# Optimization experiments

Hardware: AMD Instinct MI355X
Metric: run time of the kernel (lower is better)

The kernel has to match this reference:

```python
import jax, jax.numpy as jnp
import numpy as np

HID = 256
NL = 4
NC = 5
SPACE = 16


def _grid_sample(feat, grid):
    # feat [B,C,H,W]; grid [B,Hg,Wg,2] in [-1,1]; bilinear, align_corners=True, zeros padding
    B, C, H, W = feat.shape
    x = (grid[..., 0] + 1.0) * 0.5 * (W - 1)
    y = (grid[..., 1] + 1.0) * 0.5 * (H - 1)
    x0f = jnp.floor(x)
    y0f = jnp.floor(y)
    wx1 = x - x0f
    wy1 = y - y0f

    def corner(yf, xf, wgt):
        valid = (xf >= 0) & (xf <= W - 1) & (yf >= 0) & (yf <= H - 1)
        xi = jnp.clip(xf, 0, W - 1).astype(jnp.int32)
        yi = jnp.clip(yf, 0, H - 1).astype(jnp.int32)
        v = jax.vmap(lambda f, yy, xx: f[:, yy, xx])(feat, yi, xi)  # [B,C,Hg,Wg]
        return v * (wgt * valid.astype(feat.dtype))[:, None]

    return (corner(y0f, x0f, (1 - wy1) * (1 - wx1))
            + corner(y0f, x0f + 1, (1 - wy1) * wx1)
            + corner(y0f + 1, x0f, wy1 * (1 - wx1))
            + corner(y0f + 1, x0f + 1, wy1 * wx1))


def _conv(x, w, b, pad):
    y = jax.lax.conv_general_dilated(x, w, (1, 1), ((pad, pad), (pad, pad)),
                                     dimension_numbers=('NCHW', 'OIHW', 'NCHW'))
    return y + b[None, :, None, None]


def _resize_ac(x, oh, ow):
    # bilinear resize with align_corners=True
    B, C, H, W = x.shape
    ys = jnp.linspace(0.0, H - 1.0, oh)
    xs = jnp.linspace(0.0, W - 1.0, ow)
    y0 = jnp.floor(ys).astype(jnp.int32)
    y1 = jnp.minimum(y0 + 1, H - 1)
    x0 = jnp.floor(xs).astype(jnp.int32)
    x1 = jnp.minimum(x0 + 1, W - 1)
    wy = (ys - y0)[None, None, :, None]
    wx = (xs - x0)[None, None, None, :]
    top = x[:, :, y0, :] * (1 - wy) + x[:, :, y1, :] * wy
    return top[:, :, :, x0] * (1 - wx) + top[:, :, :, x1] * wx


def _mlp(x, w1, b1, w2, b2):
    # 2-layer MLP, dropout is identity at inference
    return jax.nn.relu(x @ w1 + b1) @ w2 + b2


def setup_inputs() -> dict:
    key = jax.random.key(0)
    ks = jax.random.split(key, 16)
    B, H, W = 8, 512, 512

    def rn(k, shape, s=0.02):
        return jax.random.normal(k, shape, jnp.float32) * s

    return {
        'images': jax.random.normal(ks[0], (B, 3, H, W), jnp.float32),
        'feat0': jax.random.normal(ks[1], (B, HID, 128, 128), jnp.float32),
        'feat1': jax.random.normal(ks[2], (B, HID, 64, 64), jnp.float32),
        'feat2': jax.random.normal(ks[3], (B, HID, 32, 32), jnp.float32),
        'feat3': jax.random.normal(ks[4], (B, HID, 16, 16), jnp.float32),
        'mask_feat': jax.random.normal(ks[5], (B, HID, 128, 128), jnp.float32),
        'o': jax.random.normal(ks[6], (B, 16, 16, 768), jnp.float32),
        'dw1': rn(ks[7], (768, HID)), 'db1': jnp.zeros((HID,), jnp.float32),
        'dw2': rn(ks[8], (HID, 8)), 'db2': jnp.zeros((8,), jnp.float32),
        'cw1': rn(ks[9], (HID, HID)), 'cb1': jnp.zeros((HID,), jnp.float32),
        'cw2': rn(ks[10], (HID, NC + 1)), 'cb2': jnp.zeros((NC + 1,), jnp.float32),
        'conv_w': rn(ks[11], (HID, HID * NL, 3, 3)), 'conv_b': jnp.zeros((HID,), jnp.float32),
        'mw1': rn(ks[12], (HID, HID, 3, 3)), 'mb1': jnp.zeros((HID,), jnp.float32),
        'bn_g': jnp.ones((HID,), jnp.float32), 'bn_b': jnp.zeros((HID,), jnp.float32),
        'bn_m': jnp.zeros((HID,), jnp.float32), 'bn_v': jnp.ones((HID,), jnp.float32),
        'mw2': rn(ks[13], (1, HID, 1, 1)), 'mb2': jnp.zeros((1,), jnp.float32),
    }


def reference(images, feat0, feat1, feat2, feat3, mask_feat, o,
              dw1, db1, dw2, db2, cw1, cb1, cw2, cb2, conv_w, conv_b,
              mw1, mb1, bn_g, bn_b, bn_m, bn_v, mw2, mb2):
    B, _, H, W = images.shape
    ny = int(np.ceil(H / SPACE))
    nx = int(np.ceil(W / SPACE))
    # AnchorPoints: meshgrid 'xy', scaled by space, shifted by half-cell origin
    gx, gy = jnp.meshgrid(jnp.arange(nx, dtype=jnp.float32), jnp.arange(ny, dtype=jnp.float32))
    origin = jnp.array([(W % SPACE) or SPACE, (H % SPACE) or SPACE], jnp.float32) / 2
    anchors = jnp.stack([gx, gy], -1) * SPACE + origin  # [ny,nx,2] (x,y)

    # learned offsets: MLP then pixel-shuffle style 16x16x8 -> 32x32x2
    d = _mlp(o, dw1, db1, dw2, db2)  # [B,16,16,8]
    d = d.reshape(B, 16, 16, 2, 2, 2).transpose(0, 1, 3, 2, 4, 5).reshape(B, 32, 32, 2)
    prop = anchors[None] + d  # deformed proposals [B,32,32,2]

    feats = [feat0, feat1, feat2, feat3]
    strides = [4, 8, 16, 32]
    rois = []
    for f, s in zip(feats, strides):
        fh, fw = f.shape[2], f.shape[3]
        grid = 2.0 * prop / s / jnp.array([fw, fh], jnp.float32) - 1.0
        rois.append(_grid_sample(f, grid))
    roi = jnp.concatenate(rois, 1)  # [B, HID*NL, 32, 32]
    roi = _conv(roi, conv_w, conv_b, 1).transpose(0, 2, 3, 1)  # [B,32,32,HID]
    logits = _mlp(roi, cw1, cb1, cw2, cb2)  # [B,32,32,NC+1]

    # mask head: conv3x3 -> BN(eval) -> ReLU -> conv1x1(pad=1) -> bilinear upsample (align_corners=True)
    m = _conv(mask_feat, mw1, mb1, 1)
    m = m * (bn_g * jax.lax.rsqrt(bn_v + 1e-5))[None, :, None, None] \
        + (bn_b - bn_m * bn_g * jax.lax.rsqrt(bn_v + 1e-5))[None, :, None, None]
    m = jax.nn.relu(m)
    m = _conv(m, mw2, mb2, 1)  # 1x1 conv with padding=1 -> [B,1,130,130] (as in source)
    masks = _resize_ac(m, H, W)  # [B,1,H,W]

    return (prop.reshape(B, -1, 2), logits.reshape(B, -1, NC + 1), masks)
```

## Files before the change

### kernel.cpp

```cpp
#include <hip/hip_runtime.h>
#include <hip/hip_bf16.h>
#include <cstdint>
#include <cstddef>

using bf16x8 = __attribute__((ext_vector_type(8))) short;
using f32x4  = __attribute__((ext_vector_type(4))) float;

static constexpr size_t ROI_OFF  = 0;
static constexpr size_t ROI_N    = (size_t)8 * 1024 * 32 * 32;
static constexpr size_t PART_OFF = ROI_OFF + ROI_N;
static constexpr size_t PART_N   = (size_t)4 * 8192 * 256;
static constexpr size_t WT_OFF   = PART_OFF + PART_N;
static constexpr size_t WTR_SH   = (size_t)294912 * 8;
static constexpr size_t WTM_SH   = (size_t)73728 * 8;
static constexpr size_t M2P_OFF  = WT_OFF + (WTR_SH + WTM_SH) / 2;
static constexpr size_t M2P_N    = (size_t)2 * 8 * 130 * 130;

__device__ __forceinline__ uint32_t pk2(float a, float b) {
  __hip_bfloat162 h = __float22bfloat162_rn(make_float2(a, b));
  union { __hip_bfloat162 h; uint32_t u; } c; c.h = h;
  return c.u;
}

__device__ __forceinline__ void gld16(const void* g, void* l) {
  __builtin_amdgcn_global_load_lds(
      (const __attribute__((address_space(1))) void*)g,
      (__attribute__((address_space(3))) void*)l, 16, 0, 0);
}

__global__ __launch_bounds__(256) void k_prep_w(
    const float* __restrict__ conv_w, const float* __restrict__ mw1,
    short* __restrict__ wTr, short* __restrict__ wTm) {
  __shared__ float sm[16 * 292];
  int t = threadIdx.x;
  int bid = blockIdx.x;
  bool is_m = (bid >= 512);
  int b2 = is_m ? (bid - 512) : bid;
  int kidx = is_m ? (b2 & 7) : (b2 & 31);
  int cog  = is_m ? (b2 >> 3) : (b2 >> 5);
  const float* src = is_m ? mw1 : conv_w;
  short* dst = is_m ? wTm : wTr;
  int CI = is_m ? 256 : 1024;
  int ci0 = kidx * 32;
  int co0 = cog * 16;
  for (int e = t; e < 4608; e += 256) {
    int row = e / 288, pos = e - row * 288;
    sm[row * 292 + pos] = src[((size_t)(co0 + row) * CI + ci0) * 9 + pos];
  }
  __syncthreads();
  int nb = cog >> 3, cofrag = cog & 7;
  for (int e = t; e < 576; e += 256) {
    int tap = e >> 6, kg = (e >> 4) & 3, lr = e & 15;
    float v[8];
#pragma unroll
    for (int j = 0; j < 8; ++j) v[j] = sm[lr * 292 + (kg * 8 + j) * 9 + tap];
    uint4 pk = make_uint4(pk2(v[0], v[1]), pk2(v[2], v[3]),
                          pk2(v[4], v[5]), pk2(v[6], v[7]));
    size_t chunk = ((size_t)(kidx * 2 + nb) * 9 + tap) * 512
                 + cofrag * 64 + kg * 16 + lr;
    *(uint4*)&dst[chunk * 8] = pk;
  }
}

__global__ __launch_bounds__(256) void k_prop(
    const float* __restrict__ o,
    const float* __restrict__ dw1, const float* __restrict__ db1,
    const float* __restrict__ dw2, const float* __restrict__ db2,
    float* __restrict__ prop) {
  __shared__ float o_lds[4 * 768];
  __shared__ float h_lds[4 * 256];
  int t = threadIdx.x;
  int bid = blockIdx.x;
  int b = bid >> 6;
  int rem = bid & 63;
  int i = rem >> 2;
  int j0 = (rem & 3) * 4;
  const float* obase = o + ((size_t)(b * 16 + i) * 16 + j0) * 768;
  for (int e = t; e < 4 * 768; e += 256) o_lds[e] = obase[e];
  __syncthreads();
  float h0 = 0.f, h1 = 0.f, h2 = 0.f, h3 = 0.f;
  for (int k = 0; k < 768; ++k) {
    float w = dw1[k * 256 + t];
    h0 = fmaf(o_lds[k], w, h0);
    h1 = fmaf(o_lds[768 + k], w, h1);
    h2 = fmaf(o_lds[1536 + k], w, h2);
    h3 = fmaf(o_lds[2304 + k], w, h3);
  }
  float bb = db1[t];
  h_lds[t]        = fmaxf(h0 + bb, 0.f);
  h_lds[256 + t]  = fmaxf(h1 + bb, 0.f);
  h_lds[512 + t]  = fmaxf(h2 + bb, 0.f);
  h_lds[768 + t]  = fmaxf(h3 + bb, 0.f);
  __syncthreads();
  if (t < 32) {
    int pos = t >> 3;
    int c   = t & 7;
    float acc = db2[c];
    const float* hp = h_lds + pos * 256;
    for (int k = 0; k < 256; ++k) acc = fmaf(hp[k], dw2[k * 8 + c], acc);
    int p = c >> 2, q = (c >> 1) & 1, cc = c & 1;
    int row = 2 * i + p;
    int col = 2 * (j0 + pos) + q;
    float anchor = (cc == 0) ? ((float)col * 16.f + 8.f) : ((float)row * 16.f + 8.f);
    prop[((size_t)(b * 32 + row) * 32 + col) * 2 + cc] = anchor + acc;
  }
}

__global__ __launch_bounds__(256) void k_sample(
    const float* __restrict__ f0, const float* __restrict__ f1,
    const float* __restrict__ f2, const float* __restrict__ f3,
    const float* __restrict__ prop, float* __restrict__ roi) {
  int py = blockIdx.x;
  int l  = blockIdx.y;
  int b  = blockIdx.z;
  int t  = threadIdx.x;
  int xq = t & 31;
  int cq = t >> 5;
  const float* f = (l == 0) ? f0 : (l == 1) ? f1 : (l == 2) ? f2 : f3;
  int fsz = 128 >> l;
  float s = (float)(4 << l);

  size_t pidx = ((size_t)b * 32 + py) * 32 + xq;
  float px = prop[pidx * 2 + 0];
  float pv = prop[pidx * 2 + 1];
  float gx = 2.f * px / s / (float)fsz - 1.f;
  float gy = 2.f * pv / s / (float)fsz - 1.f;
  float x = (gx + 1.f) * 0.5f * (float)(fsz - 1);
  float y = (gy + 1.f) * 0.5f * (float)(fsz - 1);
  float x0f = floorf(x), y0f = floorf(y);
  float wx1 = x - x0f, wy1 = y - y0f;

  int off[4];
  float wgt[4];
#pragma unroll
  for (int cy = 0; cy < 2; ++cy) {
#pragma unroll
    for (int cx = 0; cx < 2; ++cx) {
      float xf = x0f + (float)cx;
      float yf = y0f + (float)cy;
      float w = (cy ? wy1 : (1.f - wy1)) * (cx ? wx1 : (1.f - wx1));
      bool valid = (xf >= 0.f) && (xf <= (float)(fsz - 1)) &&
                   (yf >= 0.f) && (yf <= (float)(fsz - 1));
      int xi = (int)fminf(fmaxf(xf, 0.f), (float)(fsz - 1));
      int yi = (int)fminf(fmaxf(yf, 0.f), (float)(fsz - 1));
      off[cy * 2 + cx] = yi * fsz + xi;
      wgt[cy * 2 + cx] = valid ? w : 0.f;
    }
  }
  const float* fb = f + (size_t)b * 256 * fsz * fsz;
  float* rb = roi + ((size_t)b * 1024 + l * 256) * 1024 + py * 32 + xq;
  for (int c0 = 0; c0 < 256; c0 += 8) {
    int c = c0 + cq;
    const float* fc = fb + (size_t)c * fsz * fsz;
    float acc = wgt[0] * fc[off[0]] + wgt[1] * fc[off[1]] +
                wgt[2] * fc[off[2]] + wgt[3] * fc[off[3]];
    rb[(size_t)c * 1024] = acc;
  }
}

__global__ __launch_bounds__(512, 2) void k_roi_mfma(
    const float* __restrict__ roi, const short* __restrict__ wTr,
    float* __restrict__ part) {
  __shared__ short A_s[2][340 * 32];
  __shared__ short B_s[4608 * 8];
  int t = threadIdx.x;
  int lane = t & 63, wv = t >> 6, wm = wv >> 1, wn = wv & 1;
  int kg = lane >> 4, lr = lane & 15;
  int bid = blockIdx.x;
  int nb = bid & 1;
  int mi = (bid >> 1) & 31;
  int b = mi >> 2, yt = mi & 3;
  int ks = bid >> 6;

  f32x4 acc[4][4];
#pragma unroll
  for (int m = 0; m < 4; ++m)
#pragma unroll
    for (int n = 0; n < 4; ++n) acc[m][n] = {0.f, 0.f, 0.f, 0.f};

  float ld[3][8];
  auto stage_load = [&](int kc) {
#pragma unroll
    for (int i = 0; i < 3; ++i) {
      int e = i * 512 + t;
      bool on = e < 1360;
      int ee = on ? e : 0;
      int px = ee % 340;
      int cg = ee / 340;
      int r = px / 34;
      int x = px - r * 34 - 1;
      int y = yt * 8 + r - 1;
      bool ok = on && (x >= 0) && (x < 32) && (y >= 0) && (y < 32);
      const float* src = roi + (((size_t)(b * 1024 + ks * 256 + kc * 32 + cg * 8)) << 10)
                             + y * 32 + x;
#pragma unroll
      for (int j = 0; j < 8; ++j) ld[i][j] = ok ? src[j << 10] : 0.f;
    }
  };
  auto stage_write = [&](int buf) {
#pragma unroll
    for (int i = 0; i < 3; ++i) {
      int e = i * 512 + t;
      if (e < 1360) {
        int px = e % 340;
        int cg = e / 340;
        uint4 pk = make_uint4(pk2(ld[i][0], ld[i][1]), pk2(ld[i][2], ld[i][3]),
                              pk2(ld[i][4], ld[i][5]), pk2(ld[i][6], ld[i][7]));
        *(uint4*)&A_s[buf][px * 32 + (((cg ^ (px >> 1)) & 3) << 3)] = pk;
      }
    }
  };
  auto issue_h1 = [&](int kc) {
    const short* s = wTr + ((size_t)((ks * 8 + kc) * 2 + nb) * 4608) * 8;
    for (int w = wv; w < 40; w += 8)
      gld16(s + ((size_t)w * 64 + lane) * 8, &B_s[w * 512]);
  };
  auto issue_h2 = [&](int kc) {
    const short* s = wTr + (((size_t)((ks * 8 + kc) * 2 + nb) * 4608 + 2560)) * 8;
    for (int w = wv; w < 32; w += 8)
      gld16(s + ((size_t)w * 64 + lane) * 8, &B_s[2560 * 8 + w * 512]);
  };

#define ROI_TAPS(T0, T1)                                                          \
  {                                                                               \
    _Pragma("unroll")                                                             \
    for (int tap = (T0); tap < (T1); ++tap) {                                     \
      int ky = tap / 3, kx = tap - ky * 3;                                        \
      bf16x8 bfr[4];                                                              \
      _Pragma("unroll")                                                           \
      for (int n = 0; n < 4; ++n)                                                 \
        bfr[n] = *(const bf16x8*)&B_s[((((tap * 8 + wn * 4 + n) * 4 + kg) * 16)   \
                                       + lr) * 8];                                \
      _Pragma("unroll")                                                           \
      for (int m = 0; m < 4; ++m) {                                               \
        int pb = wm * 64 + m * 16;                                                \
        int px = ((pb >> 5) + ky) * 34 + (pb & 31) + lr + kx;                     \
        bf16x8 af = *(const bf16x8*)&As[px * 32 + (((kg ^ (px >> 1)) & 3) << 3)]; \
        _Pragma("unroll")                                                         \
        for (int n = 0; n < 4; ++n)                                               \
          acc[m][n] = __builtin_amdgcn_mfma_f32_16x16x32_bf16(af, bfr[n],         \
                                                              acc[m][n], 0, 0, 0);\
      }                                                                           \
    }                                                                             \
  }

  issue_h1(0);
  stage_load(0);
  stage_write(0);
  __syncthreads();

  for (int kc = 0; kc < 8; ++kc) {
    int buf = kc & 1;
    const short* As = A_s[buf];
    issue_h2(kc);
    if (kc < 7) stage_load(kc + 1);
    ROI_TAPS(0, 5);
    __syncthreads();
    if (kc < 7) { issue_h1(kc + 1); stage_write(buf ^ 1); }
    ROI_TAPS(5, 9);
    __syncthreads();
  }
#pragma unroll
  for (int m = 0; m < 4; ++m)
#pragma unroll
    for (int r = 0; r < 4; ++r) {
      int p = wm * 64 + m * 16 + kg * 4 + r;
      int y = yt * 8 + (p >> 5), x = p & 31;
      float* dst = part + (size_t)ks * 2097152 + (((size_t)b * 32 + y) * 32 + x) * 256
                        + nb * 128 + wn * 64 + lr;
#pragma unroll
      for (int n = 0; n < 4; ++n) dst[n * 16] = acc[m][n][r];
    }
}

__global__ __launch_bounds__(256) void k_mlp(
    const float* __restrict__ part, const float* __restrict__ conv_b,
    const float* __restrict__ cw1, const float* __restrict__ cb1,
    const float* __restrict__ cw2, const float* __restrict__ cb2,
    float* __restrict__ logits) {
  __shared__ float v[1024];
  __shared__ float h[1024];
  int t = threadIdx.x;
  size_t base = (size_t)blockIdx.x * 1024;
  const size_t CH = (size_t)8192 * 256;
  for (int e = t; e < 1024; e += 256) {
    float s = part[base + e] + part[CH + base + e] +
              part[2 * CH + base + e] + part[3 * CH + base + e];
    v[e] = s + conv_b[e & 255];
  }
  __syncthreads();
  float a0 = cb1[t], a1 = a0, a2 = a0, a3 = a0;
  for (int k = 0; k < 256; ++k) {
    float w = cw1[k * 256 + t];
    a0 = fmaf(v[k], w, a0);
    a1 = fmaf(v[256 + k], w, a1);
    a2 = fmaf(v[512 + k], w, a2);
    a3 = fmaf(v[768 + k], w, a3);
  }
  h[t]       = fmaxf(a0, 0.f);
  h[256 + t] = fmaxf(a1, 0.f);
  h[512 + t] = fmaxf(a2, 0.f);
  h[768 + t] = fmaxf(a3, 0.f);
  __syncthreads();
  if (t < 24) {
    int pos = t / 6, c = t - 6 * pos;
    float acc = cb2[c];
    const float* hp = h + pos * 256;
    for (int k = 0; k < 256; ++k) acc = fmaf(hp[k], cw2[k * 6 + c], acc);
    logits[((size_t)blockIdx.x * 4 + pos) * 6 + c] = acc;
  }
}

__global__ __launch_bounds__(512, 2) void k_mask_mfma(
    const float* __restrict__ mf, const short* __restrict__ wTm,
    const float* __restrict__ mb1,
    const float* __restrict__ bn_g, const float* __restrict__ bn_b,
    const float* __restrict__ bn_m, const float* __restrict__ bn_v,
    const float* __restrict__ mw2, float* __restrict__ m2p) {
  __shared__ short A_s[2][520 * 32];
  __shared__ short B_s[4608 * 8];
  int t = threadIdx.x;
  int lane = t & 63, wv = t >> 6, wm = wv >> 1, wn = wv & 1;
  int kg = lane >> 4, lr = lane & 15;
  int bid = blockIdx.x;
  int nb = bid & 1;
  int tile = bid >> 1;
  int b = tile >> 6, yt = tile & 63;

  f32x4 acc[4][4];
#pragma unroll
  for (int m = 0; m < 4; ++m)
#pragma unroll
    for (int n = 0; n < 4; ++n) acc[m][n] = {0.f, 0.f, 0.f, 0.f};

  float ld[5][8];
  auto stage_load = [&](int kc) {
#pragma unroll
    for (int i = 0; i < 5; ++i) {
      int e = i * 512 + t;
      bool on = e < 2080;
      int ee = on ? e : 0;
      int px = ee % 520;
      int cg = ee / 520;
      int r = px / 130;
      int x = px - r * 130 - 1;
      int y = 2 * yt + r - 1;
      bool ok = on && (x >= 0) && (x < 128) && (y >= 0) && (y < 128);
      const float* src = mf + (((size_t)(b * 256 + kc * 32 + cg * 8)) << 14) + y * 128 + x;
#pragma unroll
      for (int j = 0; j < 8; ++j) ld[i][j] = ok ? src[j << 14] : 0.f;
    }
  };
  auto stage_write = [&](int buf) {
#pragma unroll
    for (int i = 0; i < 5; ++i) {
      int e = i * 512 + t;
      if (e < 2080) {
        int px = e % 520;
        int cg = e / 520;
        uint4 pk = make_uint4(pk2(ld[i][0], ld[i][1]), pk2(ld[i][2], ld[i][3]),
                              pk2(ld[i][4], ld[i][5]), pk2(ld[i][6], ld[i][7]));
        *(uint4*)&A_s[buf][px * 32 + (((cg ^ (px >> 1)) & 3) << 3)] = pk;
      }
    }
  };
  auto issue_h1 = [&](int kc) {
    const short* s = wTm + ((size_t)(kc * 2 + nb) * 4608) * 8;
    for (int w = wv; w < 40; w += 8)
      gld16(s + ((size_t)w * 64 + lane) * 8, &B_s[w * 512]);
  };
  auto issue_h2 = [&](int kc) {
    const short* s = wTm + (((size_t)(kc * 2 + nb) * 4608 + 2560)) * 8;
    for (int w = wv; w < 32; w += 8)
      gld16(s + ((size_t)w * 64 + lane) * 8, &B_s[2560 * 8 + w * 512]);
  };

#define MSK_TAPS(T0, T1)                                                          \
  {                                                                               \
    _Pragma("unroll")                                                             \
    for (int tap = (T0); tap < (T1); ++tap) {                                     \
      int ky = tap / 3, kx = tap - ky * 3;                                        \
      bf16x8 bfr[4];                                                              \
      _Pragma("unroll")                                                           \
      for (int n = 0; n < 4; ++n)                                                 \
        bfr[n] = *(const bf16x8*)&B_s[((((tap * 8 + wn * 4 + n) * 4 + kg) * 16)   \
                                       + lr) * 8];                                \
      _Pragma("unroll")                                                           \
      for (int m = 0; m < 4; ++m) {                                               \
        int px = ((wm >> 1) + ky) * 130 + (wm & 1) * 64 + m * 16 + lr + kx;       \
        bf16x8 af = *(const bf16x8*)&As[px * 32 + (((kg ^ (px >> 1)) & 3) << 3)]; \
        _Pragma("unroll")                                                         \
        for (int n = 0; n < 4; ++n)                                               \
          acc[m][n] = __builtin_amdgcn_mfma_f32_16x16x32_bf16(af, bfr[n],         \
                                                              acc[m][n], 0, 0, 0);\
      }                                                                           \
    }                                                                             \
  }

  issue_h1(0);
  stage_load(0);
  stage_write(0);
  __syncthreads();

  for (int kc = 0; kc < 8; ++kc) {
    int buf = kc & 1;
    const short* As = A_s[buf];
    issue_h2(kc);
    if (kc < 7) stage_load(kc + 1);
    MSK_TAPS(0, 5);
    __syncthreads();
    if (kc < 7) { issue_h1(kc + 1); stage_write(buf ^ 1); }
    MSK_TAPS(5, 9);
    __syncthreads();
  }

  float sc[4], sh[4], w2v[4], b1[4];
#pragma unroll
  for (int n = 0; n < 4; ++n) {
    int co = nb * 128 + wn * 64 + n * 16 + lr;
    float s = bn_g[co] * rsqrtf(bn_v[co] + 1e-5f);
    sc[n] = s;
    sh[n] = bn_b[co] - bn_m[co] * s;
    b1[n] = mb1[co];
    w2v[n] = mw2[co];
  }
  float* red = (float*)&A_s[0][0];
#pragma unroll
  for (int m = 0; m < 4; ++m)
#pragma unroll
    for (int r = 0; r < 4; ++r) {
      int p = (wm >> 1) * 128 + (wm & 1) * 64 + m * 16 + kg * 4 + r;
      float s = 0.f;
#pragma unroll
      for (int n = 0; n < 4; ++n) {
        float z = fmaf(acc[m][n][r] + b1[n], sc[n], sh[n]);
        s = fmaf(w2v[n], fmaxf(z, 0.f), s);
      }
      red[p * 32 + wn * 16 + lr] = s;
    }
  __syncthreads();
  if (t < 256) {
    float s = 0.f;
#pragma unroll
    for (int q = 0; q < 32; ++q) s += red[t * 32 + q];
    int y = 2 * yt + (t >> 7);
    int x = t & 127;
    m2p[(size_t)nb * 135200 + ((size_t)b * 130 + y + 1) * 130 + x + 1] = s;
  }
}

__global__ __launch_bounds__(256) void k_resize(const float* __restrict__ m2p,
                                                const float* __restrict__ mb2,
                                                float* __restrict__ masks) {
  int idx = blockIdx.x * 256 + threadIdx.x;
  int b = idx >> 18;
  int rem = idx & 262143;
  int y = rem >> 9;
  int x = rem & 511;
  const float SC = 129.0f / 511.0f;
  float sy = (float)y * SC;
  float sx = (float)x * SC;
  float y0f = floorf(sy), x0f = floorf(sx);
  int y0 = (int)y0f, x0 = (int)x0f;
  int y1 = min(y0 + 1, 129), x1 = min(x0 + 1, 129);
  float wy = sy - y0f, wx = sx - x0f;
  float base = mb2[0];
  const float* p0 = m2p + (size_t)b * 16900;
  const float* p1 = m2p + 135200 + (size_t)b * 16900;

  auto corner = [&](int yy, int xx) -> float {
    if (yy >= 1 && yy <= 128 && xx >= 1 && xx <= 128) {
      int o2 = yy * 130 + xx;
      return base + p0[o2] + p1[o2];
    }
    return base;
  };
  float tv = corner(y0, x0) * (1.f - wx) + corner(y0, x1) * wx;
  float bv = corner(y1, x0) * (1.f - wx) + corner(y1, x1) * wx;
  masks[idx] = tv * (1.f - wy) + bv * wy;
}

extern "C" void kernel_launch(void* const* d_in, const int* in_sizes, int n_in,
                              void* d_out, int out_size, void* d_ws, size_t ws_size,
                              hipStream_t stream) {
  (void)in_sizes; (void)n_in; (void)out_size; (void)ws_size;
  const float* f0        = (const float*)d_in[1];
  const float* f1        = (const float*)d_in[2];
  const float* f2        = (const float*)d_in[3];
  const float* f3        = (const float*)d_in[4];
  const float* mask_feat = (const float*)d_in[5];
  const float* o         = (const float*)d_in[6];
  const float* dw1       = (const float*)d_in[7];
  const float* db1       = (const float*)d_in[8];
  const float* dw2       = (const float*)d_in[9];
  const float* db2       = (const float*)d_in[10];
  const float* cw1       = (const float*)d_in[11];
  const float* cb1       = (const float*)d_in[12];
  const float* cw2       = (const float*)d_in[13];
  const float* cb2       = (const float*)d_in[14];
  const float* conv_w    = (const float*)d_in[15];
  const float* conv_b    = (const float*)d_in[16];
  const float* mw1       = (const float*)d_in[17];
  const float* mb1       = (const float*)d_in[18];
  const float* bn_g      = (const float*)d_in[19];
  const float* bn_b      = (const float*)d_in[20];
  const float* bn_m      = (const float*)d_in[21];
  const float* bn_v      = (const float*)d_in[22];
  const float* mw2       = (const float*)d_in[23];
  const float* mb2       = (const float*)d_in[24];

  float* ws   = (float*)d_ws;
  float* roi  = ws + ROI_OFF;
  float* part = ws + PART_OFF;
  short* wTr  = (short*)(ws + WT_OFF);
  short* wTm  = wTr + WTR_SH;
  float* m2p  = ws + M2P_OFF;

  float* out_prop   = (float*)d_out;
  float* out_logits = out_prop + (size_t)8 * 1024 * 2;
  float* out_masks  = out_logits + (size_t)8 * 1024 * 6;

  hipLaunchKernelGGL(k_prep_w, dim3(640), dim3(256), 0, stream,
                     conv_w, mw1, wTr, wTm);
  hipLaunchKernelGGL(k_prop, dim3(512), dim3(256), 0, stream,
                     o, dw1, db1, dw2, db2, out_prop);
  hipLaunchKernelGGL(k_sample, dim3(32, 4, 8), dim3(256), 0, stream,
                     f0, f1, f2, f3, out_prop, roi);
  hipLaunchKernelGGL(k_roi_mfma, dim3(256), dim3(512), 0, stream,
                     roi, wTr, part);
  hipLaunchKernelGGL(k_mlp, dim3(2048), dim3(256), 0, stream,
                     part, conv_b, cw1, cb1, cw2, cb2, out_logits);
  hipLaunchKernelGGL(k_mask_mfma, dim3(1024), dim3(512), 0, stream,
                     mask_feat, wTm, mb1, bn_g, bn_b, bn_m, bn_v, mw2, m2p);
  hipLaunchKernelGGL(k_resize, dim3(8192), dim3(256), 0, stream,
                     m2p, mb2, out_masks);
}
```

Before: 375.8 us.

## Pre-pack activations to bf16 channel-group layout and stream via direct LDS loads

k_sample now writes the ROI features as packed bf16 in an 8-channel-group layout. A new k_cvt kernel converts mask_feat the same way into a shared workspace buffer. Both MFMA conv kernels then fill their A tiles with global_load_lds 16-byte copies, using a zeroed pad slot at chunk index -1 for out-of-bounds taps, in place of register-staged fp32 loads plus conversion. This halves activation bytes read in the conv kernels and frees registers, at the cost of an extra conversion pass over mask_feat and a reworked m2p layout without padding.

```diff
diff --git a/kernel.cpp b/kernel.cpp
--- a/kernel.cpp
+++ b/kernel.cpp
@@ -6,15 +6,11 @@
 using bf16x8 = __attribute__((ext_vector_type(8))) short;
 using f32x4  = __attribute__((ext_vector_type(4))) float;
 
-static constexpr size_t ROI_OFF  = 0;
-static constexpr size_t ROI_N    = (size_t)8 * 1024 * 32 * 32;
-static constexpr size_t PART_OFF = ROI_OFF + ROI_N;
-static constexpr size_t PART_N   = (size_t)4 * 8192 * 256;
-static constexpr size_t WT_OFF   = PART_OFF + PART_N;
+static constexpr size_t PART_OFF = 4194308;
+static constexpr size_t WT_OFF   = 16777220;
 static constexpr size_t WTR_SH   = (size_t)294912 * 8;
 static constexpr size_t WTM_SH   = (size_t)73728 * 8;
 static constexpr size_t M2P_OFF  = WT_OFF + (WTR_SH + WTM_SH) / 2;
-static constexpr size_t M2P_N    = (size_t)2 * 8 * 130 * 130;
 
 __device__ __forceinline__ uint32_t pk2(float a, float b) {
   __hip_bfloat162 h = __float22bfloat162_rn(make_float2(a, b));
@@ -30,10 +26,11 @@
 
 __global__ __launch_bounds__(256) void k_prep_w(
     const float* __restrict__ conv_w, const float* __restrict__ mw1,
-    short* __restrict__ wTr, short* __restrict__ wTm) {
+    short* __restrict__ wTr, short* __restrict__ wTm, float* __restrict__ zp) {
   __shared__ float sm[16 * 292];
   int t = threadIdx.x;
   int bid = blockIdx.x;
+  if (bid == 0 && t < 4) zp[t] = 0.f;
   bool is_m = (bid >= 512);
   int b2 = is_m ? (bid - 512) : bid;
   int kidx = is_m ? (b2 & 7) : (b2 & 31);
@@ -109,7 +106,7 @@
 __global__ __launch_bounds__(256) void k_sample(
     const float* __restrict__ f0, const float* __restrict__ f1,
     const float* __restrict__ f2, const float* __restrict__ f3,
-    const float* __restrict__ prop, float* __restrict__ roi) {
+    const float* __restrict__ prop, uint4* __restrict__ bfR) {
   int py = blockIdx.x;
   int l  = blockIdx.y;
   int b  = blockIdx.z;
@@ -148,21 +145,39 @@
     }
   }
   const float* fb = f + (size_t)b * 256 * fsz * fsz;
-  float* rb = roi + ((size_t)b * 1024 + l * 256) * 1024 + py * 32 + xq;
-  for (int c0 = 0; c0 < 256; c0 += 8) {
-    int c = c0 + cq;
-    const float* fc = fb + (size_t)c * fsz * fsz;
-    float acc = wgt[0] * fc[off[0]] + wgt[1] * fc[off[1]] +
-                wgt[2] * fc[off[2]] + wgt[3] * fc[off[3]];
-    rb[(size_t)c * 1024] = acc;
-  }
+#pragma unroll
+  for (int i = 0; i < 4; ++i) {
+    int cgl = i * 8 + cq;
+    float v[8];
+#pragma unroll
+    for (int j = 0; j < 8; ++j) {
+      const float* fc = fb + (size_t)(cgl * 8 + j) * fsz * fsz;
+      v[j] = wgt[0] * fc[off[0]] + wgt[1] * fc[off[1]] +
+             wgt[2] * fc[off[2]] + wgt[3] * fc[off[3]];
+    }
+    bfR[(((size_t)b * 128 + l * 32 + cgl) * 32 + py) * 32 + xq] =
+        make_uint4(pk2(v[0], v[1]), pk2(v[2], v[3]),
+                   pk2(v[4], v[5]), pk2(v[6], v[7]));
+  }
+}
+
+__global__ __launch_bounds__(256) void k_cvt(const float* __restrict__ mf,
+                                             uint4* __restrict__ bfA) {
+  int d = blockIdx.x * 256 + threadIdx.x;
+  int x = d & 127, y = (d >> 7) & 127, cg = (d >> 14) & 31, b = d >> 19;
+  const float* src = mf + (((size_t)(b * 256 + cg * 8)) << 14) + (y << 7) + x;
+  float v[8];
+#pragma unroll
+  for (int j = 0; j < 8; ++j) v[j] = src[(size_t)j << 14];
+  bfA[d] = make_uint4(pk2(v[0], v[1]), pk2(v[2], v[3]),
+                      pk2(v[4], v[5]), pk2(v[6], v[7]));
 }
 
 __global__ __launch_bounds__(512, 2) void k_roi_mfma(
-    const float* __restrict__ roi, const short* __restrict__ wTr,
+    const uint4* __restrict__ bfR, const short* __restrict__ wTr,
     float* __restrict__ part) {
-  __shared__ short A_s[2][340 * 32];
-  __shared__ short B_s[4608 * 8];
+  __shared__ __align__(16) short A_s[2][1408 * 8];
+  __shared__ __align__(16) short B_s[4608 * 8];
   int t = threadIdx.x;
   int lane = t & 63, wv = t >> 6, wm = wv >> 1, wn = wv & 1;
   int kg = lane >> 4, lr = lane & 15;
@@ -178,35 +193,21 @@
 #pragma unroll
     for (int n = 0; n < 4; ++n) acc[m][n] = {0.f, 0.f, 0.f, 0.f};
 
-  float ld[3][8];
-  auto stage_load = [&](int kc) {
+  auto issue_A = [&](int buf, int kc) {
 #pragma unroll
     for (int i = 0; i < 3; ++i) {
-      int e = i * 512 + t;
-      bool on = e < 1360;
-      int ee = on ? e : 0;
-      int px = ee % 340;
-      int cg = ee / 340;
-      int r = px / 34;
-      int x = px - r * 34 - 1;
-      int y = yt * 8 + r - 1;
-      bool ok = on && (x >= 0) && (x < 32) && (y >= 0) && (y < 32);
-      const float* src = roi + (((size_t)(b * 1024 + ks * 256 + kc * 32 + cg * 8)) << 10)
-                             + y * 32 + x;
-#pragma unroll
-      for (int j = 0; j < 8; ++j) ld[i][j] = ok ? src[j << 10] : 0.f;
-    }
-  };
-  auto stage_write = [&](int buf) {
-#pragma unroll
-    for (int i = 0; i < 3; ++i) {
-      int e = i * 512 + t;
-      if (e < 1360) {
-        int px = e % 340;
-        int cg = e / 340;
-        uint4 pk = make_uint4(pk2(ld[i][0], ld[i][1]), pk2(ld[i][2], ld[i][3]),
-                              pk2(ld[i][4], ld[i][5]), pk2(ld[i][6], ld[i][7]));
-        *(uint4*)&A_s[buf][px * 32 + (((cg ^ (px >> 1)) & 3) << 3)] = pk;
+      int wq = wv + 8 * i;
+      if (wq < 22) {
+        int c = wq * 64 + lane;
+        int pxi = c >> 2, slot = c & 3;
+        int r = pxi / 34;
+        int x = pxi - r * 34 - 1;
+        int y = yt * 8 + r - 1;
+        int cg4 = slot ^ ((pxi >> 1) & 3);
+        bool ok = (r < 10) && (x >= 0) && (x < 32) && (y >= 0) && (y < 32);
+        long chunk = ok ? (long)((((b * 128 + ks * 32 + kc * 4 + cg4) * 32 + y) * 32) + x)
+                        : -1L;
+        gld16(bfR + chunk, &A_s[buf][wq * 512]);
       }
     }
   };
@@ -235,7 +236,7 @@
       for (int m = 0; m < 4; ++m) {                                               \
         int pb = wm * 64 + m * 16;                                                \
         int px = ((pb >> 5) + ky) * 34 + (pb & 31) + lr + kx;                     \
-        bf16x8 af = *(const bf16x8*)&As[px * 32 + (((kg ^ (px >> 1)) & 3) << 3)]; \
+        bf16x8 af = *(const bf16x8*)&As[(px * 4 + ((kg ^ (px >> 1)) & 3)) * 8];   \
         _Pragma("unroll")                                                         \
         for (int n = 0; n < 4; ++n)                                               \
           acc[m][n] = __builtin_amdgcn_mfma_f32_16x16x32_bf16(af, bfr[n],         \
@@ -245,18 +246,17 @@
   }
 
   issue_h1(0);
-  stage_load(0);
-  stage_write(0);
+  issue_A(0, 0);
   __syncthreads();
 
   for (int kc = 0; kc < 8; ++kc) {
     int buf = kc & 1;
     const short* As = A_s[buf];
+    if (kc < 7) issue_A(buf ^ 1, kc + 1);
     issue_h2(kc);
-    if (kc < 7) stage_load(kc + 1);
     ROI_TAPS(0, 5);
     __syncthreads();
-    if (kc < 7) { issue_h1(kc + 1); stage_write(buf ^ 1); }
+    if (kc < 7) issue_h1(kc + 1);
     ROI_TAPS(5, 9);
     __syncthreads();
   }
@@ -312,13 +312,13 @@
 }
 
 __global__ __launch_bounds__(512, 2) void k_mask_mfma(
-    const float* __restrict__ mf, const short* __restrict__ wTm,
+    const uint4* __restrict__ bfA, const short* __restrict__ wTm,
     const float* __restrict__ mb1,
     const float* __restrict__ bn_g, const float* __restrict__ bn_b,
     const float* __restrict__ bn_m, const float* __restrict__ bn_v,
     const float* __restrict__ mw2, float* __restrict__ m2p) {
-  __shared__ short A_s[2][520 * 32];
-  __shared__ short B_s[4608 * 8];
+  __shared__ __align__(16) short A_s[2][2112 * 8];
+  __shared__ __align__(16) short B_s[4608 * 8];
   int t = threadIdx.x;
   int lane = t & 63, wv = t >> 6, wm = wv >> 1, wn = wv & 1;
   int kg = lane >> 4, lr = lane & 15;
@@ -333,34 +333,21 @@
 #pragma unroll
     for (int n = 0; n < 4; ++n) acc[m][n] = {0.f, 0.f, 0.f, 0.f};
 
-  float ld[5][8];
-  auto stage_load = [&](int kc) {
+  auto issue_A = [&](int buf, int kc) {
 #pragma unroll
     for (int i = 0; i < 5; ++i) {
-      int e = i * 512 + t;
-      bool on = e < 2080;
-      int ee = on ? e : 0;
-      int px = ee % 520;
-      int cg = ee / 520;
-      int r = px / 130;
-      int x = px - r * 130 - 1;
-      int y = 2 * yt + r - 1;
-      bool ok = on && (x >= 0) && (x < 128) && (y >= 0) && (y < 128);
-      const float* src = mf + (((size_t)(b * 256 + kc * 32 + cg * 8)) << 14) + y * 128 + x;
-#pragma unroll
-      for (int j = 0; j < 8; ++j) ld[i][j] = ok ? src[j << 14] : 0.f;
-    }
-  };
-  auto stage_write = [&](int buf) {
-#pragma unroll
-    for (int i = 0; i < 5; ++i) {
-      int e = i * 512 + t;
-      if (e < 2080) {
-        int px = e % 520;
-        int cg = e / 520;
-        uint4 pk = make_uint4(pk2(ld[i][0], ld[i][1]), pk2(ld[i][2], ld[i][3]),
-                              pk2(ld[i][4], ld[i][5]), pk2(ld[i][6], ld[i][7]));
-        *(uint4*)&A_s[buf][px * 32 + (((cg ^ (px >> 1)) & 3) << 3)] = pk;
+      int wq = wv + 8 * i;
+      if (wq < 33) {
+        int c = wq * 64 + lane;
+        int pxi = c >> 2, slot = c & 3;
+        int r = pxi / 130;
+        int x = pxi - r * 130 - 1;
+        int y = 2 * yt + r - 1;
+        int cg4 = slot ^ ((pxi >> 1) & 3);
+        bool ok = (r < 4) && (x >= 0) && (x < 128) && (y >= 0) && (y < 128);
+        long chunk = ok ? (long)((((b * 32 + kc * 4 + cg4) * 128 + y) * 128) + x)
+                        : -1L;
+        gld16(bfA + chunk, &A_s[buf][wq * 512]);
       }
     }
   };
@@ -388,7 +375,7 @@
       _Pragma("unroll")                                                           \
       for (int m = 0; m < 4; ++m) {                                               \
         int px = ((wm >> 1) + ky) * 130 + (wm & 1) * 64 + m * 16 + lr + kx;       \
-        bf16x8 af = *(const bf16x8*)&As[px * 32 + (((kg ^ (px >> 1)) & 3) << 3)]; \
+        bf16x8 af = *(const bf16x8*)&As[(px * 4 + ((kg ^ (px >> 1)) & 3)) * 8];   \
         _Pragma("unroll")                                                         \
         for (int n = 0; n < 4; ++n)                                               \
           acc[m][n] = __builtin_amdgcn_mfma_f32_16x16x32_bf16(af, bfr[n],         \
@@ -398,18 +385,17 @@
   }
 
   issue_h1(0);
-  stage_load(0);
-  stage_write(0);
+  issue_A(0, 0);
   __syncthreads();
 
   for (int kc = 0; kc < 8; ++kc) {
     int buf = kc & 1;
     const short* As = A_s[buf];
+    if (kc < 7) issue_A(buf ^ 1, kc + 1);
     issue_h2(kc);
-    if (kc < 7) stage_load(kc + 1);
     MSK_TAPS(0, 5);
     __syncthreads();
-    if (kc < 7) { issue_h1(kc + 1); stage_write(buf ^ 1); }
+    if (kc < 7) issue_h1(kc + 1);
     MSK_TAPS(5, 9);
     __syncthreads();
   }
@@ -445,7 +431,7 @@
     for (int q = 0; q < 32; ++q) s += red[t * 32 + q];
     int y = 2 * yt + (t >> 7);
     int x = t & 127;
-    m2p[(size_t)nb * 135200 + ((size_t)b * 130 + y + 1) * 130 + x + 1] = s;
+    m2p[(size_t)nb * 131072 + ((size_t)b * 128 + y) * 128 + x] = s;
   }
 }
 
@@ -465,12 +451,12 @@
   int y1 = min(y0 + 1, 129), x1 = min(x0 + 1, 129);
   float wy = sy - y0f, wx = sx - x0f;
   float base = mb2[0];
-  const float* p0 = m2p + (size_t)b * 16900;
-  const float* p1 = m2p + 135200 + (size_t)b * 16900;
+  const float* p0 = m2p + (size_t)b * 16384;
+  const float* p1 = m2p + 131072 + (size_t)b * 16384;
 
   auto corner = [&](int yy, int xx) -> float {
     if (yy >= 1 && yy <= 128 && xx >= 1 && xx <= 128) {
-      int o2 = yy * 130 + xx;
+      int o2 = (yy - 1) * 128 + (xx - 1);
       return base + p0[o2] + p1[o2];
     }
     return base;
@@ -510,7 +496,7 @@
   const float* mb2       = (const float*)d_in[24];
 
   float* ws   = (float*)d_ws;
-  float* roi  = ws + ROI_OFF;
+  uint4* bf   = (uint4*)(ws + 4);
   float* part = ws + PART_OFF;
   short* wTr  = (short*)(ws + WT_OFF);
   short* wTm  = wTr + WTR_SH;
@@ -521,17 +507,19 @@
   float* out_masks  = out_logits + (size_t)8 * 1024 * 6;
 
   hipLaunchKernelGGL(k_prep_w, dim3(640), dim3(256), 0, stream,
-                     conv_w, mw1, wTr, wTm);
+                     conv_w, mw1, wTr, wTm, ws);
   hipLaunchKernelGGL(k_prop, dim3(512), dim3(256), 0, stream,
                      o, dw1, db1, dw2, db2, out_prop);
   hipLaunchKernelGGL(k_sample, dim3(32, 4, 8), dim3(256), 0, stream,
-                     f0, f1, f2, f3, out_prop, roi);
+                     f0, f1, f2, f3, out_prop, bf);
   hipLaunchKernelGGL(k_roi_mfma, dim3(256), dim3(512), 0, stream,
-                     roi, wTr, part);
+                     bf, wTr, part);
   hipLaunchKernelGGL(k_mlp, dim3(2048), dim3(256), 0, stream,
                      part, conv_b, cw1, cb1, cw2, cb2, out_logits);
+  hipLaunchKernelGGL(k_cvt, dim3(16384), dim3(256), 0, stream,
+                     mask_feat, bf);
   hipLaunchKernelGGL(k_mask_mfma, dim3(1024), dim3(512), 0, stream,
-                     mask_feat, wTm, mb1, bn_g, bn_b, bn_m, bn_v, mw2, m2p);
+                     bf, wTm, mb1, bn_g, bn_b, bn_m, bn_v, mw2, m2p);
   hipLaunchKernelGGL(k_resize, dim3(8192), dim3(256), 0, stream,
                      m2p, mb2, out_masks);
 }
```

Measured after the change: 352.1 us. -6.3%, faster.
